# Kernel optimization log

Hardware: AMD Instinct MI355X
Metric: run time of the kernel (lower is better)

Reference implementation:

```python
import jax, jax.numpy as jnp
from jax import lax
import numpy as np

BN_EPS = 1e-5

def _bn(x, g, b, m, v):
    # inference-mode BatchNorm1d (running stats)
    return (x - m) * (g / jnp.sqrt(v + BN_EPS)) + b

def _mlp2(x, W1, g, b, m, v, W2):
    # Linear(no bias) -> BN -> ReLU -> (Dropout off in eval) -> Linear(no bias)
    h = jax.nn.relu(_bn(x @ W1.T, g, b, m, v))
    return h @ W2.T

def setup_inputs() -> dict:
    key = jax.random.key(0)
    ks = iter(jax.random.split(key, 40))
    B, N = 1024, 10
    f32 = jnp.float32
    def w(shape, s=0.02):
        return jax.random.normal(next(ks), shape, f32) * s
    def bn_params(c):
        return (jnp.ones((c,), f32), jnp.zeros((c,), f32),
                jax.random.normal(next(ks), (c,), f32) * 0.1,
                jax.random.uniform(next(ks), (c,), f32, 0.5, 1.5))
    inp = {
        'features_object': jax.random.normal(next(ks), (B, N, 1024), f32),
        'bbox': jax.random.uniform(next(ks), (B, N, 4), f32),
        'word_embedding': jax.random.normal(next(ks), (B, N, 300), f32),
        'sentiment': jax.random.normal(next(ks), (B, N, 4096), f32),
        'body': jax.random.normal(next(ks), (B, 2048), f32),
    }
    # mlp_object: 1024 -> 128 -> 128
    inp['W1_o'] = w((128, 1024)); inp['g_o'], inp['b_o'], inp['m_o'], inp['v_o'] = bn_params(128)
    inp['W2_o'] = w((128, 128))
    # mlp_sentiment: 4096 -> 512 -> 128
    inp['W1_s'] = w((512, 4096)); inp['g_s'], inp['b_s'], inp['m_s'], inp['v_s'] = bn_params(512)
    inp['W2_s'] = w((128, 512))
    # mlp_body: 2048 -> 256 -> 128
    inp['W1_b'] = w((256, 2048)); inp['g_b'], inp['b_b'], inp['m_b'], inp['v_b'] = bn_params(256)
    inp['W2_b'] = w((128, 256))
    # channel attention (CBAM-style, in_planes=10, ratio=2): shared MLP 10->5->10
    inp['Wc1'] = w((5, 10), 0.3)
    inp['Wc2'] = w((10, 5), 0.3)
    # spatial attention: Conv1d(2 -> 1, k=7, pad=3, no bias)
    inp['Wsa'] = w((1, 2, 7), 0.3)
    # fc1: 688 -> 256 (with bias) then BN
    inp['Wf'] = w((256, 688)); inp['bf'] = jnp.zeros((256,), f32)
    inp['g_f'], inp['b_f'], inp['m_f'], inp['v_f'] = bn_params(256)
    return inp

def reference(features_object, bbox, word_embedding, sentiment, body,
              W1_o, g_o, b_o, m_o, v_o, W2_o,
              W1_s, g_s, b_s, m_s, v_s, W2_s,
              W1_b, g_b, b_b, m_b, v_b, W2_b,
              Wc1, Wc2, Wsa, Wf, bf, g_f, b_f, m_f, v_f):
    B, N, _ = features_object.shape
    # per-slice MLPs batched into single GEMMs over B*N rows
    obj = _mlp2(features_object.reshape(B * N, -1), W1_o, g_o, b_o, m_o, v_o, W2_o).reshape(B, N, 128)
    sen = _mlp2(sentiment.reshape(B * N, -1), W1_s, g_s, b_s, m_s, v_s, W2_s).reshape(B, N, 128)
    # body is identical across the N repeats (inference BN), compute once and broadcast
    bod = _mlp2(body.reshape(B, -1), W1_b, g_b, b_b, m_b, v_b, W2_b)
    bod = jnp.broadcast_to(bod[:, None, :], (B, N, 128))
    x = jnp.concatenate([obj, bbox, word_embedding, sen, bod], axis=2)  # [B,N,688]
    # channel attention over the N-slice axis
    def ca_mlp(a):  # [B,N] -> [B,N]
        return jax.nn.relu(a @ Wc1.T) @ Wc2.T
    att_c = jax.nn.sigmoid(ca_mlp(x.mean(axis=2)) + ca_mlp(x.max(axis=2)))  # [B,N]
    x = x * att_c[:, :, None]
    # spatial attention along feature axis
    s = jnp.stack([x.mean(axis=1), x.max(axis=1)], axis=1)  # [B,2,688]
    sa = lax.conv_general_dilated(s, Wsa, (1,), [(3, 3)],
                                  dimension_numbers=('NCH', 'OIH', 'NCH'))  # [B,1,688]
    x = x * jax.nn.sigmoid(sa)
    x = x.sum(axis=1)  # [B,688]
    out = jax.nn.relu(_bn(x @ Wf.T + bf, g_f, b_f, m_f, v_f))  # [B,256]
    return out
```

## Files before the change

kernel.cpp:

```cpp
#include <hip/hip_runtime.h>
#include <hip/hip_bf16.h>
#include <math.h>

typedef __attribute__((ext_vector_type(8))) short short8;
typedef __attribute__((ext_vector_type(4))) float floatx4;

static __device__ __forceinline__ unsigned short f2bf(float f) {
    unsigned int u = __float_as_uint(f);
    unsigned int r = (u + 0x7fffu + ((u >> 16) & 1u)) >> 16;
    return (unsigned short)r;
}

static __device__ __forceinline__ void g2l16(const void* g, void* l) {
    __builtin_amdgcn_global_load_lds(
        (const __attribute__((address_space(1))) unsigned int*)g,
        (__attribute__((address_space(3))) unsigned int*)l,
        16, 0, 0);
}

struct GDesc {
    const float*          Af;
    const unsigned short* Ab;
    const unsigned short* W;
    float*          Cf;
    unsigned short* Cb;
    const float *bias, *g, *b, *m, *v;
    int M, N, K;
    int Kreal;
    int fuse;
    int nbx;
    int block0;
    int nbb;
    int ksplit;
};
struct GArgs { GDesc g[3]; int n; };

__global__ __launch_bounds__(256)
void gemm_grouped(GArgs ga)
{
    __shared__ unsigned short As[2][4096];
    __shared__ unsigned short Bs[2][4096];

    const int bid = blockIdx.x;
    int gi = 0;
    #pragma unroll
    for (int i = 1; i < 3; ++i)
        if (i < ga.n && bid >= ga.g[i].block0) gi = i;
    const GDesc d = ga.g[gi];

    int local = bid - d.block0;
    int kc = 0;
    int Kc = d.K;
    if (d.ksplit > 1) {
        Kc = d.K / d.ksplit;
        kc = local / d.nbb;
        local -= kc * d.nbb;
    }
    const int kbeg = kc * Kc;
    const int bx = local % d.nbx;
    const int by = local / d.nbx;
    const int row0 = by * 128;
    const int col0 = bx * 128;

    const int tid  = threadIdx.x;
    const int wave = tid >> 6;
    const int lane = tid & 63;
    const int qd   = lane >> 4;
    const int ln   = lane & 15;
    const int wr   = (wave >> 1) * 64;
    const int wc   = (wave & 1) * 64;

    const int c0 = wave * 128 + lane;
    const int c1 = c0 + 64;
    const int r0 = c0 >> 2, k0 = (c0 & 3) * 8;
    const int r1 = c1 >> 2, k1 = (c1 & 3) * 8;

    const int sr = tid >> 3;
    const int sc = (tid & 7) * 4;

    const bool afp = (d.Af != nullptr);
    const int niter = Kc >> 5;

    floatx4 acc[4][4];
    #pragma unroll
    for (int i = 0; i < 4; ++i)
        #pragma unroll
        for (int j = 0; j < 4; ++j) acc[i][j] = (floatx4){0.f, 0.f, 0.f, 0.f};

    g2l16(d.W + (size_t)(col0 + r0) * d.K + kbeg + k0, &Bs[0][(size_t)wave * 1024]);
    g2l16(d.W + (size_t)(col0 + r1) * d.K + kbeg + k1, &Bs[0][(size_t)wave * 1024 + 512]);
    if (afp) {
        #pragma unroll
        for (int p = 0; p < 4; ++p) {
            float4 v = (kbeg + sc < d.Kreal)
                ? *(const float4*)(d.Af + (size_t)(row0 + p * 32 + sr) * d.Kreal + kbeg + sc)
                : (float4){0.f, 0.f, 0.f, 0.f};
            ushort4 o = { f2bf(v.x), f2bf(v.y), f2bf(v.z), f2bf(v.w) };
            *(ushort4*)&As[0][(p * 32 + sr) * 32 + sc] = o;
        }
    } else {
        g2l16(d.Ab + (size_t)(row0 + r0) * d.K + kbeg + k0, &As[0][(size_t)wave * 1024]);
        g2l16(d.Ab + (size_t)(row0 + r1) * d.K + kbeg + k1, &As[0][(size_t)wave * 1024 + 512]);
    }
    __syncthreads();

    int cur = 0;
    for (int it = 0; it < niter; ++it) {
        const int kk = it * 32;
        const int nxt = cur ^ 1;
        const bool pf = (it + 1 < niter);

        float4 areg[4];
        if (pf) {
            const int kg = kbeg + kk + 32;
            g2l16(d.W + (size_t)(col0 + r0) * d.K + kg + k0, &Bs[nxt][(size_t)wave * 1024]);
            g2l16(d.W + (size_t)(col0 + r1) * d.K + kg + k1, &Bs[nxt][(size_t)wave * 1024 + 512]);
            if (afp) {
                #pragma unroll
                for (int p = 0; p < 4; ++p)
                    areg[p] = (kg + sc < d.Kreal)
                        ? *(const float4*)(d.Af + (size_t)(row0 + p * 32 + sr) * d.Kreal + kg + sc)
                        : (float4){0.f, 0.f, 0.f, 0.f};
            } else {
                g2l16(d.Ab + (size_t)(row0 + r0) * d.K + kg + k0, &As[nxt][(size_t)wave * 1024]);
                g2l16(d.Ab + (size_t)(row0 + r1) * d.K + kg + k1, &As[nxt][(size_t)wave * 1024 + 512]);
            }
        }

        short8 a[4], b[4];
        #pragma unroll
        for (int i = 0; i < 4; ++i)
            a[i] = *(const short8*)&As[cur][(wr + i * 16 + ln) * 32 + qd * 8];
        #pragma unroll
        for (int j = 0; j < 4; ++j)
            b[j] = *(const short8*)&Bs[cur][(wc + j * 16 + ln) * 32 + qd * 8];
        #pragma unroll
        for (int i = 0; i < 4; ++i)
            #pragma unroll
            for (int j = 0; j < 4; ++j)
                acc[i][j] = __builtin_amdgcn_mfma_f32_16x16x32_bf16(
                                a[i], b[j], acc[i][j], 0, 0, 0);

        if (pf && afp) {
            #pragma unroll
            for (int p = 0; p < 4; ++p) {
                ushort4 o = { f2bf(areg[p].x), f2bf(areg[p].y),
                              f2bf(areg[p].z), f2bf(areg[p].w) };
                *(ushort4*)&As[nxt][(p * 32 + sr) * 32 + sc] = o;
            }
        }
        __syncthreads();
        cur = nxt;
    }

    if (d.ksplit > 1) {
        #pragma unroll
        for (int j = 0; j < 4; ++j) {
            const int col = col0 + wc + j * 16 + ln;
            #pragma unroll
            for (int i = 0; i < 4; ++i) {
                #pragma unroll
                for (int r = 0; r < 4; ++r) {
                    const int row = row0 + wr + i * 16 + qd * 4 + r;
                    atomicAdd(&d.Cf[(size_t)row * d.N + col], acc[i][j][r]);
                }
            }
        }
        return;
    }

    #pragma unroll
    for (int j = 0; j < 4; ++j) {
        const int col = col0 + wc + j * 16 + ln;
        float add = d.bias ? d.bias[col] : 0.f;
        float scale = 1.f, shift = 0.f;
        if (d.fuse) {
            scale = d.g[col] * rsqrtf(d.v[col] + 1e-5f);
            shift = d.b[col] - d.m[col] * scale;
        }
        #pragma unroll
        for (int i = 0; i < 4; ++i) {
            #pragma unroll
            for (int r = 0; r < 4; ++r) {
                const int row = row0 + wr + i * 16 + qd * 4 + r;
                float vv = acc[i][j][r] + add;
                if (d.fuse) vv = fmaxf(vv * scale + shift, 0.f);
                if (d.Cf) d.Cf[(size_t)row * d.N + col] = vv;
                if (d.Cb) d.Cb[(size_t)row * d.N + col] = f2bf(vv);
            }
        }
    }
}

struct WSeg { const float* src; unsigned short* dst; int Kreal; int Kp; };
struct WArgs { WSeg s[7]; int off[8]; };

__global__ __launch_bounds__(256)
void cvt_weights(WArgs wa)
{
    int i = blockIdx.x * 256 + threadIdx.x;
    if (i >= wa.off[7]) return;
    int s = 0;
    #pragma unroll
    for (int j = 1; j < 7; ++j) if (i >= wa.off[j]) s = j;
    const WSeg sg = wa.s[s];
    const int li = i - wa.off[s];
    const int r = li / sg.Kp, c = li - r * sg.Kp;
    sg.dst[li] = (c < sg.Kreal) ? f2bf(sg.src[(size_t)r * sg.Kreal + c])
                                : (unsigned short)0;
}

struct FSeg { const float* src; unsigned short* dst;
              const float *g, *b, *m, *v; int N; };
struct FArgs { FSeg s[3]; int off[4]; };

__global__ __launch_bounds__(256)
void bn_finalize(FArgs fa)
{
    int i = blockIdx.x * 256 + threadIdx.x;
    if (i >= fa.off[3]) return;
    int s = 0;
    #pragma unroll
    for (int j = 1; j < 3; ++j) if (i >= fa.off[j]) s = j;
    const FSeg sg = fa.s[s];
    const int li = i - fa.off[s];
    const int e = li * 4;
    const int col = e % sg.N;
    float4 vv = *(const float4*)(sg.src + e);
    ushort4 o;
    #pragma unroll
    for (int r = 0; r < 4; ++r) {
        float sc = sg.g[col + r] * rsqrtf(sg.v[col + r] + 1e-5f);
        float sh = sg.b[col + r] - sg.m[col + r] * sc;
        float x  = fmaxf((&vv.x)[r] * sc + sh, 0.f);
        ((unsigned short*)&o)[r] = f2bf(x);
    }
    *(ushort4*)(sg.dst + e) = o;
}

__global__ __launch_bounds__(256)
void attn_kernel(const float* __restrict__ obj, const float* __restrict__ bbox,
                 const float* __restrict__ word, const float* __restrict__ sen,
                 const float* __restrict__ bod,
                 const float* __restrict__ Wc1, const float* __restrict__ Wc2,
                 const float* __restrict__ Wsa,
                 float* __restrict__ xsum_out)
{
    const int b = blockIdx.x;
    const int tid = threadIdx.x;

    __shared__ float xs[10][688];
    __shared__ float s0[688], s1[688];
    __shared__ float avec[10], mvec[10], att[10];
    __shared__ float cw[14], c1[50], c2[50];

    if (tid < 14) cw[tid] = Wsa[tid];
    if (tid < 50) { c1[tid] = Wc1[tid]; c2[tid] = Wc2[tid]; }

    for (int n = 0; n < 10; ++n) {
        const float* o  = obj  + ((size_t)b * 10 + n) * 128;
        const float* bx = bbox + ((size_t)b * 10 + n) * 4;
        const float* w  = word + ((size_t)b * 10 + n) * 300;
        const float* s  = sen  + ((size_t)b * 10 + n) * 128;
        const float* bo = bod  + (size_t)b * 128;
        for (int c = tid; c < 688; c += 256) {
            float v;
            if      (c < 128) v = o[c];
            else if (c < 132) v = bx[c - 128];
            else if (c < 432) v = w[c - 132];
            else if (c < 560) v = s[c - 432];
            else              v = bo[c - 560];
            xs[n][c] = v;
        }
    }
    __syncthreads();

    if (tid < 10) {
        float sm = 0.f, mx = -INFINITY;
        for (int c = 0; c < 688; ++c) {
            float v = xs[tid][c];
            sm += v; mx = fmaxf(mx, v);
        }
        avec[tid] = sm * (1.f / 688.f);
        mvec[tid] = mx;
    }
    __syncthreads();

    if (tid == 0) {
        float ha[5], hm[5];
        #pragma unroll
        for (int i = 0; i < 5; ++i) {
            float sa_ = 0.f, sm_ = 0.f;
            #pragma unroll
            for (int j = 0; j < 10; ++j) {
                sa_ += c1[i * 10 + j] * avec[j];
                sm_ += c1[i * 10 + j] * mvec[j];
            }
            ha[i] = fmaxf(sa_, 0.f);
            hm[i] = fmaxf(sm_, 0.f);
        }
        #pragma unroll
        for (int j = 0; j < 10; ++j) {
            float v = 0.f;
            #pragma unroll
            for (int i = 0; i < 5; ++i) v += c2[j * 5 + i] * (ha[i] + hm[i]);
            att[j] = 1.f / (1.f + expf(-v));
        }
    }
    __syncthreads();

    for (int c = tid; c < 688; c += 256) {
        float sm = 0.f, mx = -INFINITY;
        #pragma unroll
        for (int n = 0; n < 10; ++n) {
            float v = xs[n][c] * att[n];
            xs[n][c] = v;
            sm += v; mx = fmaxf(mx, v);
        }
        s0[c] = sm * 0.1f;
        s1[c] = mx;
    }
    __syncthreads();

    for (int c = tid; c < 688; c += 256) {
        float sa = 0.f;
        #pragma unroll
        for (int j = 0; j < 7; ++j) {
            int cc = c + j - 3;
            if (cc >= 0 && cc < 688)
                sa += cw[j] * s0[cc] + cw[7 + j] * s1[cc];
        }
        float sig = 1.f / (1.f + expf(-sa));
        float sm = 0.f;
        #pragma unroll
        for (int n = 0; n < 10; ++n) sm += xs[n][c];
        xsum_out[(size_t)b * 688 + c] = sm * sig;
    }
}

extern "C" void kernel_launch(void* const* d_in, const int* in_sizes, int n_in,
                              void* d_out, int out_size, void* d_ws, size_t ws_size,
                              hipStream_t stream)
{
    const float* f_obj = (const float*)d_in[0];
    const float* bbox  = (const float*)d_in[1];
    const float* word  = (const float*)d_in[2];
    const float* sent  = (const float*)d_in[3];
    const float* body  = (const float*)d_in[4];
    const float* W1_o  = (const float*)d_in[5];
    const float* g_o = (const float*)d_in[6],  *b_o = (const float*)d_in[7];
    const float* m_o = (const float*)d_in[8],  *v_o = (const float*)d_in[9];
    const float* W2_o  = (const float*)d_in[10];
    const float* W1_s  = (const float*)d_in[11];
    const float* g_s = (const float*)d_in[12], *b_s = (const float*)d_in[13];
    const float* m_s = (const float*)d_in[14], *v_s = (const float*)d_in[15];
    const float* W2_s  = (const float*)d_in[16];
    const float* W1_b  = (const float*)d_in[17];
    const float* g_b = (const float*)d_in[18], *b_b = (const float*)d_in[19];
    const float* m_b = (const float*)d_in[20], *v_b = (const float*)d_in[21];
    const float* W2_b  = (const float*)d_in[22];
    const float* Wc1 = (const float*)d_in[23];
    const float* Wc2 = (const float*)d_in[24];
    const float* Wsa = (const float*)d_in[25];
    const float* Wf  = (const float*)d_in[26];
    const float* bf  = (const float*)d_in[27];
    const float* g_f = (const float*)d_in[28], *b_f = (const float*)d_in[29];
    const float* m_f = (const float*)d_in[30], *v_f = (const float*)d_in[31];
    float* out = (float*)d_out;

    char* p = (char*)d_ws;
    unsigned short* w1s = (unsigned short*)p; p += 4194304;
    unsigned short* w2s = (unsigned short*)p; p += 131072;
    unsigned short* w1o = (unsigned short*)p; p += 262144;
    unsigned short* w2o = (unsigned short*)p; p += 32768;
    unsigned short* w1b = (unsigned short*)p; p += 1048576;
    unsigned short* w2b = (unsigned short*)p; p += 65536;
    unsigned short* wfp = (unsigned short*)p; p += 360448;
    unsigned short* h_s = (unsigned short*)p; p += 10485760;
    unsigned short* h_o = (unsigned short*)p; p += 2621440;
    unsigned short* h_b = (unsigned short*)p; p += 524288;
    char* region = p; p += 27262976;
    float* ps = (float*)region;
    float* po = (float*)(region + 20971520);
    float* pb = (float*)(region + 26214400);
    float* sen_f  = (float*)region;
    float* obj_f  = (float*)(region + 5242880);
    float* bod_f  = (float*)(region + 10485760);
    float* xsum_f = (float*)(region + 11010048);
    if ((size_t)(p - (char*)d_ws) > ws_size) return;

    hipMemsetAsync(region, 0, 27262976, stream);

    WArgs wa;
    wa.s[0] = { W1_s, w1s, 4096, 4096 };
    wa.s[1] = { W2_s, w2s,  512,  512 };
    wa.s[2] = { W1_o, w1o, 1024, 1024 };
    wa.s[3] = { W2_o, w2o,  128,  128 };
    wa.s[4] = { W1_b, w1b, 2048, 2048 };
    wa.s[5] = { W2_b, w2b,  256,  256 };
    wa.s[6] = { Wf,   wfp,  688,  704 };
    const int wn[7] = { 512*4096, 128*512, 128*1024, 128*128, 256*2048, 128*256, 256*704 };
    wa.off[0] = 0;
    for (int i = 0; i < 7; ++i) wa.off[i + 1] = wa.off[i] + wn[i];
    cvt_weights<<<(wa.off[7] + 255) / 256, 256, 0, stream>>>(wa);

    {
        GArgs ga; ga.n = 3;
        ga.g[0] = { sent,  nullptr, w1s, ps, nullptr, nullptr, nullptr, nullptr, nullptr, nullptr,
                    10240, 512, 4096, 4096, 0, 4, 0,   320, 2 };
        ga.g[1] = { f_obj, nullptr, w1o, po, nullptr, nullptr, nullptr, nullptr, nullptr, nullptr,
                    10240, 128, 1024, 1024, 0, 1, 640, 80,  2 };
        ga.g[2] = { body,  nullptr, w1b, pb, nullptr, nullptr, nullptr, nullptr, nullptr, nullptr,
                    1024,  256, 2048, 2048, 0, 2, 800, 16,  2 };
        gemm_grouped<<<832, 256, 0, stream>>>(ga);
    }

    {
        FArgs fa;
        fa.s[0] = { ps, h_s, g_s, b_s, m_s, v_s, 512 };
        fa.s[1] = { po, h_o, g_o, b_o, m_o, v_o, 128 };
        fa.s[2] = { pb, h_b, g_b, b_b, m_b, v_b, 256 };
        fa.off[0] = 0;
        fa.off[1] = 10240 * 512 / 4;
        fa.off[2] = fa.off[1] + 10240 * 128 / 4;
        fa.off[3] = fa.off[2] + 1024 * 256 / 4;
        bn_finalize<<<(fa.off[3] + 255) / 256, 256, 0, stream>>>(fa);
    }

    {
        GArgs ga; ga.n = 3;
        ga.g[0] = { nullptr, h_s, w2s, sen_f, nullptr, nullptr, nullptr, nullptr, nullptr, nullptr,
                    10240, 128, 512, 512, 0, 1, 0,   80, 1 };
        ga.g[1] = { nullptr, h_o, w2o, obj_f, nullptr, nullptr, nullptr, nullptr, nullptr, nullptr,
                    10240, 128, 128, 128, 0, 1, 80,  80, 1 };
        ga.g[2] = { nullptr, h_b, w2b, bod_f, nullptr, nullptr, nullptr, nullptr, nullptr, nullptr,
                    1024,  128, 256, 256, 0, 1, 160, 8,  1 };
        gemm_grouped<<<168, 256, 0, stream>>>(ga);
    }

    attn_kernel<<<1024, 256, 0, stream>>>(obj_f, bbox, word, sen_f, bod_f,
                                          Wc1, Wc2, Wsa, xsum_f);

    {
        GArgs ga; ga.n = 1;
        ga.g[0] = { xsum_f, nullptr, wfp, out, nullptr, bf, g_f, b_f, m_f, v_f,
                    1024, 256, 704, 688, 1, 2, 0, 16, 1 };
        gemm_grouped<<<16, 256, 0, stream>>>(ga);
    }
}
```

Before: 528.2 us.

## Raise split-K across all GEMMs, deepen A prefetch, parallelize attention reductions

The fp32 A-operand prefetch now runs two iterations ahead, with the bf16 conversion and LDS store moved before the MFMA block. Split-K factors go up for the first-layer, second-layer and final fc GEMMs, giving more blocks. The fused fc epilogue moves into a separate bn_finalize pass with bias support, and a second memset clears the atomic targets. The per-slice mean and max in the attention kernel become wave-parallel shuffle reductions instead of 10 serial threads. The cost is more atomic traffic and extra launches and memsets.

```diff
diff --git a/kernel.cpp b/kernel.cpp
--- a/kernel.cpp
+++ b/kernel.cpp
@@ -89,6 +89,7 @@
 
     g2l16(d.W + (size_t)(col0 + r0) * d.K + kbeg + k0, &Bs[0][(size_t)wave * 1024]);
     g2l16(d.W + (size_t)(col0 + r1) * d.K + kbeg + k1, &Bs[0][(size_t)wave * 1024 + 512]);
+    float4 areg[4];
     if (afp) {
         #pragma unroll
         for (int p = 0; p < 4; ++p) {
@@ -98,6 +99,14 @@
             ushort4 o = { f2bf(v.x), f2bf(v.y), f2bf(v.z), f2bf(v.w) };
             *(ushort4*)&As[0][(p * 32 + sr) * 32 + sc] = o;
         }
+        if (niter > 1) {
+            const int kg = kbeg + 32;
+            #pragma unroll
+            for (int p = 0; p < 4; ++p)
+                areg[p] = (kg + sc < d.Kreal)
+                    ? *(const float4*)(d.Af + (size_t)(row0 + p * 32 + sr) * d.Kreal + kg + sc)
+                    : (float4){0.f, 0.f, 0.f, 0.f};
+        }
     } else {
         g2l16(d.Ab + (size_t)(row0 + r0) * d.K + kbeg + k0, &As[0][(size_t)wave * 1024]);
         g2l16(d.Ab + (size_t)(row0 + r1) * d.K + kbeg + k1, &As[0][(size_t)wave * 1024 + 512]);
@@ -106,21 +115,28 @@
 
     int cur = 0;
     for (int it = 0; it < niter; ++it) {
-        const int kk = it * 32;
         const int nxt = cur ^ 1;
         const bool pf = (it + 1 < niter);
 
-        float4 areg[4];
         if (pf) {
-            const int kg = kbeg + kk + 32;
+            const int kg = kbeg + (it + 1) * 32;
             g2l16(d.W + (size_t)(col0 + r0) * d.K + kg + k0, &Bs[nxt][(size_t)wave * 1024]);
             g2l16(d.W + (size_t)(col0 + r1) * d.K + kg + k1, &Bs[nxt][(size_t)wave * 1024 + 512]);
             if (afp) {
                 #pragma unroll
-                for (int p = 0; p < 4; ++p)
-                    areg[p] = (kg + sc < d.Kreal)
-                        ? *(const float4*)(d.Af + (size_t)(row0 + p * 32 + sr) * d.Kreal + kg + sc)
-                        : (float4){0.f, 0.f, 0.f, 0.f};
+                for (int p = 0; p < 4; ++p) {
+                    ushort4 o = { f2bf(areg[p].x), f2bf(areg[p].y),
+                                  f2bf(areg[p].z), f2bf(areg[p].w) };
+                    *(ushort4*)&As[nxt][(p * 32 + sr) * 32 + sc] = o;
+                }
+                if (it + 2 < niter) {
+                    const int kg2 = kbeg + (it + 2) * 32;
+                    #pragma unroll
+                    for (int p = 0; p < 4; ++p)
+                        areg[p] = (kg2 + sc < d.Kreal)
+                            ? *(const float4*)(d.Af + (size_t)(row0 + p * 32 + sr) * d.Kreal + kg2 + sc)
+                            : (float4){0.f, 0.f, 0.f, 0.f};
+                }
             } else {
                 g2l16(d.Ab + (size_t)(row0 + r0) * d.K + kg + k0, &As[nxt][(size_t)wave * 1024]);
                 g2l16(d.Ab + (size_t)(row0 + r1) * d.K + kg + k1, &As[nxt][(size_t)wave * 1024 + 512]);
@@ -141,14 +157,6 @@
                 acc[i][j] = __builtin_amdgcn_mfma_f32_16x16x32_bf16(
                                 a[i], b[j], acc[i][j], 0, 0, 0);
 
-        if (pf && afp) {
-            #pragma unroll
-            for (int p = 0; p < 4; ++p) {
-                ushort4 o = { f2bf(areg[p].x), f2bf(areg[p].y),
-                              f2bf(areg[p].z), f2bf(areg[p].w) };
-                *(ushort4*)&As[nxt][(p * 32 + sr) * 32 + sc] = o;
-            }
-        }
         __syncthreads();
         cur = nxt;
     }
@@ -210,8 +218,8 @@
                                 : (unsigned short)0;
 }
 
-struct FSeg { const float* src; unsigned short* dst;
-              const float *g, *b, *m, *v; int N; };
+struct FSeg { const float* src; unsigned short* dstb; float* dstf;
+              const float *bias, *g, *b, *m, *v; int N; };
 struct FArgs { FSeg s[3]; int off[4]; };
 
 __global__ __launch_bounds__(256)
@@ -227,15 +235,20 @@
     const int e = li * 4;
     const int col = e % sg.N;
     float4 vv = *(const float4*)(sg.src + e);
+    float4 fo;
     ushort4 o;
     #pragma unroll
     for (int r = 0; r < 4; ++r) {
+        float x = (&vv.x)[r];
+        if (sg.bias) x += sg.bias[col + r];
         float sc = sg.g[col + r] * rsqrtf(sg.v[col + r] + 1e-5f);
         float sh = sg.b[col + r] - sg.m[col + r] * sc;
-        float x  = fmaxf((&vv.x)[r] * sc + sh, 0.f);
+        x = fmaxf(x * sc + sh, 0.f);
+        (&fo.x)[r] = x;
         ((unsigned short*)&o)[r] = f2bf(x);
     }
-    *(ushort4*)(sg.dst + e) = o;
+    if (sg.dstb) *(ushort4*)(sg.dstb + e) = o;
+    if (sg.dstf) *(float4*)(sg.dstf + e) = fo;
 }
 
 __global__ __launch_bounds__(256)
@@ -275,14 +288,21 @@
     }
     __syncthreads();
 
-    if (tid < 10) {
-        float sm = 0.f, mx = -INFINITY;
-        for (int c = 0; c < 688; ++c) {
-            float v = xs[tid][c];
-            sm += v; mx = fmaxf(mx, v);
-        }
-        avec[tid] = sm * (1.f / 688.f);
-        mvec[tid] = mx;
+    {
+        const int wv = tid >> 6, ln2 = tid & 63;
+        for (int n = wv; n < 10; n += 4) {
+            float sm = 0.f, mx = -INFINITY;
+            for (int c = ln2; c < 688; c += 64) {
+                float v = xs[n][c];
+                sm += v; mx = fmaxf(mx, v);
+            }
+            #pragma unroll
+            for (int off = 32; off > 0; off >>= 1) {
+                sm += __shfl_down(sm, off);
+                mx = fmaxf(mx, __shfl_down(mx, off));
+            }
+            if (ln2 == 0) { avec[n] = sm * (1.f / 688.f); mvec[n] = mx; }
+        }
     }
     __syncthreads();
 
@@ -386,7 +406,8 @@
     float* sen_f  = (float*)region;
     float* obj_f  = (float*)(region + 5242880);
     float* bod_f  = (float*)(region + 10485760);
-    float* xsum_f = (float*)(region + 11010048);
+    float* pf     = (float*)(region + 11010048);
+    float* xsum_f = (float*)(region + 12058624);
     if ((size_t)(p - (char*)d_ws) > ws_size) return;
 
     hipMemsetAsync(region, 0, 27262976, stream);
@@ -407,19 +428,19 @@
     {
         GArgs ga; ga.n = 3;
         ga.g[0] = { sent,  nullptr, w1s, ps, nullptr, nullptr, nullptr, nullptr, nullptr, nullptr,
-                    10240, 512, 4096, 4096, 0, 4, 0,   320, 2 };
+                    10240, 512, 4096, 4096, 0, 4, 0,    320, 4 };
         ga.g[1] = { f_obj, nullptr, w1o, po, nullptr, nullptr, nullptr, nullptr, nullptr, nullptr,
-                    10240, 128, 1024, 1024, 0, 1, 640, 80,  2 };
+                    10240, 128, 1024, 1024, 0, 1, 1280, 80,  4 };
         ga.g[2] = { body,  nullptr, w1b, pb, nullptr, nullptr, nullptr, nullptr, nullptr, nullptr,
-                    1024,  256, 2048, 2048, 0, 2, 800, 16,  2 };
-        gemm_grouped<<<832, 256, 0, stream>>>(ga);
+                    1024,  256, 2048, 2048, 0, 2, 1600, 16,  4 };
+        gemm_grouped<<<1664, 256, 0, stream>>>(ga);
     }
 
     {
         FArgs fa;
-        fa.s[0] = { ps, h_s, g_s, b_s, m_s, v_s, 512 };
-        fa.s[1] = { po, h_o, g_o, b_o, m_o, v_o, 128 };
-        fa.s[2] = { pb, h_b, g_b, b_b, m_b, v_b, 256 };
+        fa.s[0] = { ps, h_s, nullptr, nullptr, g_s, b_s, m_s, v_s, 512 };
+        fa.s[1] = { po, h_o, nullptr, nullptr, g_o, b_o, m_o, v_o, 128 };
+        fa.s[2] = { pb, h_b, nullptr, nullptr, g_b, b_b, m_b, v_b, 256 };
         fa.off[0] = 0;
         fa.off[1] = 10240 * 512 / 4;
         fa.off[2] = fa.off[1] + 10240 * 128 / 4;
@@ -427,15 +448,17 @@
         bn_finalize<<<(fa.off[3] + 255) / 256, 256, 0, stream>>>(fa);
     }
 
+    hipMemsetAsync(region, 0, 12058624, stream);
+
     {
         GArgs ga; ga.n = 3;
         ga.g[0] = { nullptr, h_s, w2s, sen_f, nullptr, nullptr, nullptr, nullptr, nullptr, nullptr,
-                    10240, 128, 512, 512, 0, 1, 0,   80, 1 };
+                    10240, 128, 512, 512, 0, 1, 0,   80, 4 };
         ga.g[1] = { nullptr, h_o, w2o, obj_f, nullptr, nullptr, nullptr, nullptr, nullptr, nullptr,
-                    10240, 128, 128, 128, 0, 1, 80,  80, 1 };
+                    10240, 128, 128, 128, 0, 1, 320, 80, 2 };
         ga.g[2] = { nullptr, h_b, w2b, bod_f, nullptr, nullptr, nullptr, nullptr, nullptr, nullptr,
-                    1024,  128, 256, 256, 0, 1, 160, 8,  1 };
-        gemm_grouped<<<168, 256, 0, stream>>>(ga);
+                    1024,  128, 256, 256, 0, 1, 480, 8,  2 };
+        gemm_grouped<<<496, 256, 0, stream>>>(ga);
     }
 
     attn_kernel<<<1024, 256, 0, stream>>>(obj_f, bbox, word, sen_f, bod_f,
@@ -443,8 +466,20 @@
 
     {
         GArgs ga; ga.n = 1;
-        ga.g[0] = { xsum_f, nullptr, wfp, out, nullptr, bf, g_f, b_f, m_f, v_f,
-                    1024, 256, 704, 688, 1, 2, 0, 16, 1 };
-        gemm_grouped<<<16, 256, 0, stream>>>(ga);
-    }
-}
+        ga.g[0] = { xsum_f, nullptr, wfp, pf, nullptr, nullptr, nullptr, nullptr, nullptr, nullptr,
+                    1024, 256, 704, 688, 0, 2, 0, 16, 11 };
+        gemm_grouped<<<176, 256, 0, stream>>>(ga);
+    }
+
+    {
+        FArgs fa;
+        fa.s[0] = { pf, nullptr, out, bf, g_f, b_f, m_f, v_f, 256 };
+        fa.s[1] = fa.s[0];
+        fa.s[2] = fa.s[0];
+        fa.off[0] = 0;
+        fa.off[1] = 1024 * 256 / 4;
+        fa.off[2] = fa.off[1];
+        fa.off[3] = fa.off[1];
+        bn_finalize<<<(fa.off[1] + 255) / 256, 256, 0, stream>>>(fa);
+    }
+}
```

Result: slower. 578.8 us (+9.6%).
